# Performance work log

Measured on AMD Instinct MI355X. Metric: run time of the kernel, lower is better.

## Reference

```python
import math
import jax, jax.numpy as jnp
import numpy as np

B, S, E, H = 1, 2048, 2048, 16
HD = E // H // 2            # qk head dim = 64
DEPTH = 12
LAMBDA_INIT = 0.8 - 0.6 * math.exp(-0.3 * DEPTH)
EPS = 1e-5
NEG = -1e30

# rotary table (non-learned buffer), interleaved pairs, dim = HD
_pos = np.arange(S, dtype=np.float32)[:, None]
_div = np.exp(np.arange(0, HD, 2, dtype=np.float32) * (-math.log(10000.0) / HD))
COS = jnp.asarray(np.cos(_pos * _div))  # [S, HD/2]
SIN = jnp.asarray(np.sin(_pos * _div))


def _rope_interleaved(x):
    # x: [B, S, nH, HD]; rotate interleaved pairs (x0,x1),(x2,x3),...
    x1 = x[..., 0::2]
    x2 = x[..., 1::2]
    c = COS[None, :, None, :]
    s = SIN[None, :, None, :]
    o1 = x1 * c - x2 * s
    o2 = x1 * s + x2 * c
    return jnp.stack([o1, o2], axis=-1).reshape(x.shape)


def _causal_attn(q, k, v):
    # q,k: [B,S,H,Dk]; v: [B,S,H,Dv]; flash_attn default scale = Dk**-0.5
    scale = q.shape[-1] ** -0.5
    scores = jnp.einsum('bqhd,bkhd->bhqk', q, k) * scale
    mask = jnp.tril(jnp.ones((S, S), dtype=bool))
    scores = jnp.where(mask[None, None], scores, NEG)
    p = jax.nn.softmax(scores, axis=-1)
    return jnp.einsum('bhqk,bkhd->bqhd', p, v)


def setup_inputs() -> dict:
    key = jax.random.key(0)
    ks = jax.random.split(key, 10)
    w = lambda k: jax.random.normal(k, (E, E), dtype=jnp.float32) * 0.02
    lam = lambda k: jax.random.normal(k, (HD,), dtype=jnp.float32) * 0.1
    return {
        'x': jax.random.normal(ks[0], (B, S, E), dtype=jnp.float32),
        'Wq': w(ks[1]), 'Wk': w(ks[2]), 'Wv': w(ks[3]), 'Wo': w(ks[4]),
        'lq1': lam(ks[5]), 'lk1': lam(ks[6]), 'lq2': lam(ks[7]), 'lk2': lam(ks[8]),
        'g': jnp.ones((2 * HD,), dtype=jnp.float32),  # RMSNorm affine weight
    }


def reference(x, Wq, Wk, Wv, Wo, lq1, lk1, lq2, lk2, g):
    q = (x @ Wq).reshape(B, S, 2 * H, HD)
    k = (x @ Wk).reshape(B, S, 2 * H, HD)
    v = (x @ Wv).reshape(B, S, H, 2 * HD)
    q = _rope_interleaved(q).reshape(B, S, H, 2, HD)
    k = _rope_interleaved(k).reshape(B, S, H, 2, HD)
    q1, q2 = q[:, :, :, 0], q[:, :, :, 1]
    k1, k2 = k[:, :, :, 0], k[:, :, :, 1]
    attn1 = _causal_attn(q1, k1, v)  # [B,S,H,2*HD]
    attn2 = _causal_attn(q2, k2, v)
    lambda_full = (jnp.exp(jnp.sum(lq1 * lk1)) - jnp.exp(jnp.sum(lq2 * lk2))
                   + LAMBDA_INIT)
    a = attn1 - lambda_full * attn2
    # RMSNorm over last dim (2*HD) with affine weight g
    a = a * jax.lax.rsqrt(jnp.mean(a * a, axis=-1, keepdims=True) + EPS) * g
    a = a * (1.0 - LAMBDA_INIT)
    a = a.reshape(B, S, E)
    return a @ Wo
```

## Files before the change

kernel.cpp:

```cpp
#include <hip/hip_runtime.h>

typedef unsigned short u16;
typedef __bf16 bf16x8 __attribute__((ext_vector_type(8)));
typedef float f32x4 __attribute__((ext_vector_type(4)));

#define LAMBDA_INIT_F 0.7836057665f
#define ONE_MINUS_LI  0.2163942335f
#define Q_PRESCALE 0.1803368801f

__device__ __forceinline__ u16 f2bf(float f) {
  union { float f; unsigned u; } v; v.f = f;
  unsigned r = v.u + 0x7fffu + ((v.u >> 16) & 1u);
  return (u16)(r >> 16);
}

__device__ __forceinline__ float fast_exp2(float x) {
#if __has_builtin(__builtin_amdgcn_exp2f)
  return __builtin_amdgcn_exp2f(x);
#else
  return __builtin_exp2f(x);
#endif
}

__device__ __forceinline__ void gload_lds16(const void* g, void* l) {
  __builtin_amdgcn_global_load_lds(
      (const __attribute__((address_space(1))) void*)g,
      (__attribute__((address_space(3))) void*)l, 16, 0, 0);
}

__global__ __launch_bounds__(256) void prep_kernel(
    const float* __restrict__ x, const float* __restrict__ Wq,
    const float* __restrict__ Wk, const float* __restrict__ Wv,
    const float* __restrict__ Wo, const float* __restrict__ lq1,
    const float* __restrict__ lk1, const float* __restrict__ lq2,
    const float* __restrict__ lk2, u16* __restrict__ xb,
    u16* __restrict__ WqkvT, u16* __restrict__ WoT,
    float* __restrict__ cosT, float* __restrict__ sinT, float* __restrict__ lam) {
  __shared__ float t[32][33];
  const int bid = blockIdx.x;
  const int tid = threadIdx.x;
  if (bid < 16384) {
    const int z = bid >> 12;
    const int rem = bid & 4095;
    const int n0 = (rem & 63) * 32, k0 = (rem >> 6) * 32;
    const float* src = (z == 0) ? Wq : (z == 1) ? Wk : (z == 2) ? Wv : Wo;
    const int tx = tid & 31, ty = tid >> 5;
#pragma unroll
    for (int i = 0; i < 4; ++i)
      t[ty + i * 8][tx] = src[(size_t)(k0 + ty + i * 8) * 2048 + n0 + tx];
    __syncthreads();
    u16* dst = (z < 3) ? (WqkvT + ((size_t)z * 2048 + n0) * 2048 + k0)
                       : (WoT + (size_t)n0 * 2048 + k0);
#pragma unroll
    for (int i = 0; i < 4; ++i)
      dst[(size_t)(ty + i * 8) * 2048 + tx] = f2bf(t[tx][ty + i * 8]);
  } else if (bid < 16384 + 4096) {
    const int i = ((bid - 16384) * 256 + tid) * 4;
    const float4 v = *(const float4*)(x + i);
    u16 tmp[4] = {f2bf(v.x), f2bf(v.y), f2bf(v.z), f2bf(v.w)};
    *(uint2*)(xb + i) = *(const uint2*)tmp;
  } else if (bid < 16384 + 4096 + 256) {
    const int idx = (bid - 16384 - 4096) * 256 + tid;
    const int s = idx >> 5, i = idx & 31;
    const float div = expf((float)(2 * i) * (-9.210340371976184f / 64.f));
    const float ang = (float)s * div;
    cosT[idx] = cosf(ang);
    sinT[idx] = sinf(ang);
  } else {
    if (tid < 64) {
      float p1 = lq1[tid] * lk1[tid];
      float p2 = lq2[tid] * lk2[tid];
#pragma unroll
      for (int mk = 1; mk < 64; mk <<= 1) {
        p1 += __shfl_xor(p1, mk);
        p2 += __shfl_xor(p2, mk);
      }
      if (tid == 0) *lam = expf(p1) - expf(p2) + LAMBDA_INIT_F;
    }
  }
}

__global__ __launch_bounds__(256) void gemm_bt_kernel(
    const u16* __restrict__ A, const u16* __restrict__ Bt,
    float* __restrict__ C, int M, int N, int K, int mode,
    const float* __restrict__ cosT, const float* __restrict__ sinT,
    u16* __restrict__ Qh, u16* __restrict__ Kh, u16* __restrict__ Vt) {
  __shared__ u16 As[2][128 * 64];
  __shared__ u16 Bs[2][128 * 64];
  const int tid = threadIdx.x;
  const int lane = tid & 63;
  const int w = tid >> 6;
  const int wm = w >> 1, wn = w & 1;
  const long m0 = (long)blockIdx.y * 128;
  const long n0 = (long)blockIdx.x * 128;

  f32x4 acc[4][4];
#pragma unroll
  for (int i = 0; i < 4; ++i)
#pragma unroll
    for (int j = 0; j < 4; ++j) acc[i][j] = f32x4{0.f, 0.f, 0.f, 0.f};

  const int sr = lane >> 3;
  const int scS = ((lane & 7) ^ sr) * 8;
  const int fr = lane & 15;
  const int kgrp = lane >> 4;
  const int swz = (fr & 7) << 3;

  const u16* aSrc = A + (m0 + w * 32 + sr) * (long)K + scS;
  const u16* bSrc = Bt + (n0 + w * 32 + sr) * (long)K + scS;

  auto stage = [&](int b, long koff) {
#pragma unroll
    for (int g = 0; g < 4; ++g) {
      gload_lds16(aSrc + koff + (size_t)g * 8 * K, &As[b][(w * 32 + g * 8) * 64]);
      gload_lds16(bSrc + koff + (size_t)g * 8 * K, &Bs[b][(w * 32 + g * 8) * 64]);
    }
  };

  stage(0, 0);
  __syncthreads();
  int cur = 0;
  for (int k0 = 0; k0 < K; k0 += 64) {
    if (k0 + 64 < K) stage(cur ^ 1, k0 + 64);
    __builtin_amdgcn_s_setprio(1);
#pragma unroll
    for (int ks = 0; ks < 2; ++ks) {
      bf16x8 af[4], bfr[4];
#pragma unroll
      for (int mi = 0; mi < 4; ++mi)
        af[mi] = *(const bf16x8*)&As[cur][(wm * 64 + mi * 16 + fr) * 64 +
                                          ((ks * 32 + kgrp * 8) ^ swz)];
#pragma unroll
      for (int ni = 0; ni < 4; ++ni)
        bfr[ni] = *(const bf16x8*)&Bs[cur][(wn * 64 + ni * 16 + fr) * 64 +
                                           ((ks * 32 + kgrp * 8) ^ swz)];
#pragma unroll
      for (int mi = 0; mi < 4; ++mi)
#pragma unroll
        for (int ni = 0; ni < 4; ++ni)
          acc[mi][ni] =
              __builtin_amdgcn_mfma_f32_16x16x32_bf16(af[mi], bfr[ni], acc[mi][ni], 0, 0, 0);
    }
    __builtin_amdgcn_s_setprio(0);
    __syncthreads();
    cur ^= 1;
  }
  const int rg = (lane >> 4) * 4;
  if (mode == 0) {
#pragma unroll
    for (int mi = 0; mi < 4; ++mi)
#pragma unroll
      for (int ni = 0; ni < 4; ++ni) {
        const long col = n0 + wn * 64 + ni * 16 + fr;
#pragma unroll
        for (int j = 0; j < 4; ++j) {
          const long row = m0 + wm * 64 + mi * 16 + rg + j;
          C[row * N + col] = acc[mi][ni][j];
        }
      }
  } else if (n0 >= 4096) {
#pragma unroll
    for (int mi = 0; mi < 4; ++mi)
#pragma unroll
      for (int ni = 0; ni < 4; ++ni) {
        const long vr = n0 - 4096 + wn * 64 + ni * 16 + fr;
#pragma unroll
        for (int j = 0; j < 4; ++j) {
          const long row = m0 + wm * 64 + mi * 16 + rg + j;
          Vt[vr * 2048 + row] = f2bf(acc[mi][ni][j]);
        }
      }
  } else {
    const int isK = (int)(n0 >> 11);
    u16* dstBase = isK ? Kh : Qh;
    const float scl = isK ? 1.0f : Q_PRESCALE;
#pragma unroll
    for (int mi = 0; mi < 4; ++mi)
#pragma unroll
      for (int ni = 0; ni < 4; ++ni) {
        const int col = (int)(n0 & 2047) + wn * 64 + ni * 16 + fr;
        const int hh = col >> 6, d = col & 63, i2 = (col & 63) >> 1;
        const bool odd = d & 1;
#pragma unroll
        for (int j = 0; j < 4; ++j) {
          const int row = (int)m0 + wm * 64 + mi * 16 + rg + j;
          const float v = acc[mi][ni][j];
          const float p = __shfl_xor(v, 1);
          const float c = cosT[row * 32 + i2], sn = sinT[row * 32 + i2];
          const float outv = odd ? (p * sn + v * c) : (v * c - p * sn);
          dstBase[((size_t)hh * 2048 + row) * 64 + d] = f2bf(outv * scl);
        }
      }
  }
}

__global__ __launch_bounds__(256) void attn_kernel(
    const u16* __restrict__ Qh, const u16* __restrict__ Kh,
    const u16* __restrict__ Vt, float* __restrict__ attnOut) {
  __shared__ u16 Kt[2][64 * 64];
  __shared__ u16 Vs[2][128 * 64];
  __shared__ __bf16 Ps[4 * 16 * 64];
  const int tid = threadIdx.x, lane = tid & 63, w = tid >> 6;
  const int fr = lane & 15, kgrp = lane >> 4;
  const int bid = blockIdx.x;
  const int xcd = bid & 7, idx = bid >> 3;
  const int hh = xcd * 4 + (idx & 3);
  const int pairIdx = idx >> 2;
  const int h = hh >> 1, comp = hh & 1;
  const int q0A = pairIdx * 64, q0B = (31 - pairIdx) * 64;
  const int jmaxA = pairIdx, jmaxB = 31 - pairIdx;
  const int ntA = jmaxA + 1, ntot = ntA + jmaxB + 1;

  const int sr = lane >> 3;
  const int scS = (((lane & 7) ^ sr) * 8);
  const int swz = (fr & 7) << 3;

  bf16x8 qf0, qf1;
  {
    const u16* qb = Qh + ((size_t)hh * 2048 + q0A + w * 16 + fr) * 64 + kgrp * 8;
    qf0 = *(const bf16x8*)qb;
    qf1 = *(const bf16x8*)(qb + 32);
  }
  bf16x8 onesf;
#pragma unroll
  for (int i = 0; i < 8; ++i) onesf[i] = (__bf16)1.0f;

  f32x4 o[9];
#pragma unroll
  for (int i = 0; i < 9; ++i) o[i] = f32x4{0.f, 0.f, 0.f, 0.f};
  float m_r[4] = {-1e30f, -1e30f, -1e30f, -1e30f};

  auto stage = [&](int b, int kv0) {
#pragma unroll
    for (int i = 0; i < 2; ++i)
      gload_lds16(Kh + ((size_t)hh * 2048 + kv0 + i * 32 + w * 8 + sr) * 64 + scS,
                  &Kt[b][(i * 32 + w * 8) * 64]);
#pragma unroll
    for (int i = 0; i < 4; ++i)
      gload_lds16(Vt + ((size_t)h * 128 + i * 32 + w * 8 + sr) * 2048 + kv0 + scS,
                  &Vs[b][(i * 32 + w * 8) * 64]);
  };

  auto writeOut = [&](int q0) {
    float* outp = attnOut + (size_t)comp * (2048 * 2048);
#pragma unroll
    for (int j = 0; j < 4; ++j) {
      const int row = q0 + w * 16 + kgrp * 4 + j;
      const float inv = 1.0f / o[8][j];
      float* op = outp + (size_t)row * 2048 + h * 128;
#pragma unroll
      for (int nf = 0; nf < 8; ++nf) op[nf * 16 + fr] = o[nf][j] * inv;
    }
  };

  stage(0, 0);
  __syncthreads();

  for (int t = 0; t < ntot; ++t) {
    const int cur = t & 1;
    if (t + 1 < ntot) {
      const int nk = (t + 1 < ntA) ? (t + 1) * 64 : (t + 1 - ntA) * 64;
      stage(cur ^ 1, nk);
    }
    const bool inA = t < ntA;
    const int q0 = inA ? q0A : q0B;
    const int jj = inA ? t : t - ntA;
    const int kv0 = jj * 64;
    const bool diag = inA ? (jj == jmaxA) : (jj == jmaxB);

    f32x4 s[4];
    __builtin_amdgcn_s_setprio(1);
#pragma unroll
    for (int nf = 0; nf < 4; ++nf) {
      s[nf] = f32x4{0.f, 0.f, 0.f, 0.f};
      const bf16x8 b0 = *(const bf16x8*)&Kt[cur][(nf * 16 + fr) * 64 + ((kgrp * 8) ^ swz)];
      const bf16x8 b1 =
          *(const bf16x8*)&Kt[cur][(nf * 16 + fr) * 64 + ((32 + kgrp * 8) ^ swz)];
      s[nf] = __builtin_amdgcn_mfma_f32_16x16x32_bf16(qf0, b0, s[nf], 0, 0, 0);
      s[nf] = __builtin_amdgcn_mfma_f32_16x16x32_bf16(qf1, b1, s[nf], 0, 0, 0);
    }
    __builtin_amdgcn_s_setprio(0);

    float pmax[4] = {-1e30f, -1e30f, -1e30f, -1e30f};
    if (diag) {
#pragma unroll
      for (int nf = 0; nf < 4; ++nf) {
        const int key = kv0 + nf * 16 + fr;
#pragma unroll
        for (int j = 0; j < 4; ++j) {
          float sc2 = s[nf][j];
          if (key > q0 + w * 16 + kgrp * 4 + j) sc2 = -1e30f;
          s[nf][j] = sc2;
          pmax[j] = fmaxf(pmax[j], sc2);
        }
      }
    } else {
#pragma unroll
      for (int nf = 0; nf < 4; ++nf)
#pragma unroll
        for (int j = 0; j < 4; ++j) pmax[j] = fmaxf(pmax[j], s[nf][j]);
    }
#pragma unroll
    for (int j = 0; j < 4; ++j)
#pragma unroll
      for (int mk = 1; mk < 16; mk <<= 1) pmax[j] = fmaxf(pmax[j], __shfl_xor(pmax[j], mk));

    bool grow = false;
#pragma unroll
    for (int j = 0; j < 4; ++j) grow |= (pmax[j] > m_r[j]);
    if (__any(grow)) {
#pragma unroll
      for (int j = 0; j < 4; ++j) {
        const float mn = fmaxf(m_r[j], pmax[j]);
        const float sf = fast_exp2(m_r[j] - mn);
        m_r[j] = mn;
#pragma unroll
        for (int nf = 0; nf < 9; ++nf) o[nf][j] *= sf;
      }
    }

#pragma unroll
    for (int nf = 0; nf < 4; ++nf)
#pragma unroll
      for (int j = 0; j < 4; ++j) {
        const float p = fast_exp2(s[nf][j] - m_r[j]);
        const int prow = kgrp * 4 + j;
        Ps[w * 1024 + prow * 64 + ((nf * 16 + fr) ^ ((prow & 7) << 3))] = (__bf16)p;
      }

    const bf16x8 pa0 = *(const bf16x8*)&Ps[w * 1024 + fr * 64 + ((kgrp * 8) ^ swz)];
    const bf16x8 pa1 = *(const bf16x8*)&Ps[w * 1024 + fr * 64 + ((32 + kgrp * 8) ^ swz)];
    __builtin_amdgcn_s_setprio(1);
#pragma unroll
    for (int nf = 0; nf < 8; ++nf) {
      const bf16x8 v0 = *(const bf16x8*)&Vs[cur][(nf * 16 + fr) * 64 + ((kgrp * 8) ^ swz)];
      const bf16x8 v1 =
          *(const bf16x8*)&Vs[cur][(nf * 16 + fr) * 64 + ((32 + kgrp * 8) ^ swz)];
      o[nf] = __builtin_amdgcn_mfma_f32_16x16x32_bf16(pa0, v0, o[nf], 0, 0, 0);
      o[nf] = __builtin_amdgcn_mfma_f32_16x16x32_bf16(pa1, v1, o[nf], 0, 0, 0);
    }
    o[8] = __builtin_amdgcn_mfma_f32_16x16x32_bf16(pa0, onesf, o[8], 0, 0, 0);
    o[8] = __builtin_amdgcn_mfma_f32_16x16x32_bf16(pa1, onesf, o[8], 0, 0, 0);
    __builtin_amdgcn_s_setprio(0);

    if (t == jmaxA) {
      writeOut(q0A);
#pragma unroll
      for (int i = 0; i < 9; ++i) o[i] = f32x4{0.f, 0.f, 0.f, 0.f};
#pragma unroll
      for (int j = 0; j < 4; ++j) m_r[j] = -1e30f;
      const u16* qb = Qh + ((size_t)hh * 2048 + q0B + w * 16 + fr) * 64 + kgrp * 8;
      qf0 = *(const bf16x8*)qb;
      qf1 = *(const bf16x8*)(qb + 32);
    }
    __syncthreads();
  }
  writeOut(q0B);
}

__global__ __launch_bounds__(256) void combine_kernel(
    const float* __restrict__ attn, const float* __restrict__ lam,
    const float* __restrict__ g, u16* __restrict__ ab) {
  const int lane = threadIdx.x & 63;
  const int idx = blockIdx.x * 4 + (threadIdx.x >> 6);
  const int s = idx >> 4, h = idx & 15;
  const float lf = *lam;
  const float* a1 = attn + (size_t)s * 2048 + h * 128;
  const float* a2 = a1 + (size_t)2048 * 2048;
  const float x0 = a1[lane] - lf * a2[lane];
  const float x1 = a1[lane + 64] - lf * a2[lane + 64];
  float ss = x0 * x0 + x1 * x1;
#pragma unroll
  for (int mk = 1; mk < 64; mk <<= 1) ss += __shfl_xor(ss, mk);
  const float r = rsqrtf(ss * (1.0f / 128.0f) + 1e-5f) * ONE_MINUS_LI;
  u16* op = ab + (size_t)s * 2048 + h * 128;
  op[lane] = f2bf(x0 * r * g[lane]);
  op[lane + 64] = f2bf(x1 * r * g[lane + 64]);
}

extern "C" void kernel_launch(void* const* d_in, const int* in_sizes, int n_in,
                              void* d_out, int out_size, void* d_ws, size_t ws_size,
                              hipStream_t stream) {
  const float* x = (const float*)d_in[0];
  const float* Wq = (const float*)d_in[1];
  const float* Wk = (const float*)d_in[2];
  const float* Wv = (const float*)d_in[3];
  const float* Wo = (const float*)d_in[4];
  const float* lq1 = (const float*)d_in[5];
  const float* lk1 = (const float*)d_in[6];
  const float* lq2 = (const float*)d_in[7];
  const float* lk2 = (const float*)d_in[8];
  const float* g = (const float*)d_in[9];
  float* out = (float*)d_out;

  char* ws = (char*)d_ws;
  u16* xb = (u16*)(ws);
  u16* WqkvT = (u16*)(ws + (size_t)(8u << 20));
  u16* WoT = (u16*)(ws + (size_t)(32u << 20));
  float* attn = (float*)(ws + (size_t)(40u << 20));
  u16* Qh = (u16*)(ws + (size_t)(88u << 20));
  u16* Kh = (u16*)(ws + (size_t)(96u << 20));
  u16* Vt = (u16*)(ws + (size_t)(104u << 20));
  u16* ab = (u16*)(ws + (size_t)(112u << 20));
  float* cosT = (float*)(ws + (size_t)(120u << 20));
  float* sinT = (float*)(ws + (size_t)(120u << 20) + (256u << 10));
  float* lam = (float*)(ws + (size_t)(120u << 20) + (512u << 10));

  prep_kernel<<<16384 + 4096 + 256 + 1, 256, 0, stream>>>(
      x, Wq, Wk, Wv, Wo, lq1, lk1, lq2, lk2, xb, WqkvT, WoT, cosT, sinT, lam);
  gemm_bt_kernel<<<dim3(48, 16), 256, 0, stream>>>(xb, WqkvT, nullptr, 2048, 6144, 2048,
                                                   1, cosT, sinT, Qh, Kh, Vt);
  attn_kernel<<<512, 256, 0, stream>>>(Qh, Kh, Vt, attn);
  combine_kernel<<<8192, 256, 0, stream>>>(attn, lam, g, ab);
  gemm_bt_kernel<<<dim3(16, 16), 256, 0, stream>>>(ab, WoT, out, 2048, 2048, 2048,
                                                   0, nullptr, nullptr, nullptr, nullptr,
                                                   nullptr);
}
```

Baseline: 316.0 us.

## Fuse differential combine and RMSNorm into attention kernel, sharing V across components

The attention kernel now runs both differential components of a head in one 512-thread block: waves 0-3 compute component 1 and waves 4-7 compute component 2, and the V tile is staged once and shared. Component 2 passes its normalized output through shared memory so component 1 can apply the lambda subtraction, RMSNorm and gain, then write bf16 directly. This removes the separate combine kernel and the 32 MB fp32 intermediate round trip, and halves V loads. In exchange the grid drops to 256 larger blocks, shared memory use rises, and block-level syncs gain extra work at the switch points.

```diff
diff --git a/kernel.cpp b/kernel.cpp
--- a/kernel.cpp
+++ b/kernel.cpp
@@ -194,30 +194,39 @@
   }
 }
 
-__global__ __launch_bounds__(256) void attn_kernel(
+__global__ __launch_bounds__(512) void attn_kernel(
     const u16* __restrict__ Qh, const u16* __restrict__ Kh,
-    const u16* __restrict__ Vt, float* __restrict__ attnOut) {
-  __shared__ u16 Kt[2][64 * 64];
+    const u16* __restrict__ Vt, const float* __restrict__ lam,
+    const float* __restrict__ g, u16* __restrict__ ab) {
+  __shared__ u16 Kt1[2][64 * 64];
+  __shared__ u16 Kt2[2][64 * 64];
   __shared__ u16 Vs[2][128 * 64];
-  __shared__ __bf16 Ps[4 * 16 * 64];
+  __shared__ __bf16 Ps[8 * 16 * 64];
+  __shared__ float Xch[4][16][132];
   const int tid = threadIdx.x, lane = tid & 63, w = tid >> 6;
+  const int comp = w >> 2, wq = w & 3;
   const int fr = lane & 15, kgrp = lane >> 4;
   const int bid = blockIdx.x;
   const int xcd = bid & 7, idx = bid >> 3;
-  const int hh = xcd * 4 + (idx & 3);
-  const int pairIdx = idx >> 2;
-  const int h = hh >> 1, comp = hh & 1;
+  const int h = xcd * 2 + (idx & 1);
+  const int pairIdx = idx >> 1;
   const int q0A = pairIdx * 64, q0B = (31 - pairIdx) * 64;
   const int jmaxA = pairIdx, jmaxB = 31 - pairIdx;
   const int ntA = jmaxA + 1, ntot = ntA + jmaxB + 1;
+  const size_t hhQ = (size_t)(2 * h + comp);
 
   const int sr = lane >> 3;
   const int scS = (((lane & 7) ^ sr) * 8);
   const int swz = (fr & 7) << 3;
 
+  const float lf = *lam;
+  float gv[8];
+#pragma unroll
+  for (int nf = 0; nf < 8; ++nf) gv[nf] = g[nf * 16 + fr];
+
   bf16x8 qf0, qf1;
   {
-    const u16* qb = Qh + ((size_t)hh * 2048 + q0A + w * 16 + fr) * 64 + kgrp * 8;
+    const u16* qb = Qh + (hhQ * 2048 + q0A + wq * 16 + fr) * 64 + kgrp * 8;
     qf0 = *(const bf16x8*)qb;
     qf1 = *(const bf16x8*)(qb + 32);
   }
@@ -231,26 +240,49 @@
   float m_r[4] = {-1e30f, -1e30f, -1e30f, -1e30f};
 
   auto stage = [&](int b, int kv0) {
+    gload_lds16(Kh + ((size_t)(2 * h) * 2048 + kv0 + w * 8 + sr) * 64 + scS,
+                &Kt1[b][(w * 8) * 64]);
+    gload_lds16(Kh + ((size_t)(2 * h + 1) * 2048 + kv0 + w * 8 + sr) * 64 + scS,
+                &Kt2[b][(w * 8) * 64]);
 #pragma unroll
     for (int i = 0; i < 2; ++i)
-      gload_lds16(Kh + ((size_t)hh * 2048 + kv0 + i * 32 + w * 8 + sr) * 64 + scS,
-                  &Kt[b][(i * 32 + w * 8) * 64]);
-#pragma unroll
-    for (int i = 0; i < 4; ++i)
-      gload_lds16(Vt + ((size_t)h * 128 + i * 32 + w * 8 + sr) * 2048 + kv0 + scS,
-                  &Vs[b][(i * 32 + w * 8) * 64]);
+      gload_lds16(Vt + ((size_t)h * 128 + w * 16 + i * 8 + sr) * 2048 + kv0 + scS,
+                  &Vs[b][(w * 16 + i * 8) * 64]);
   };
 
-  auto writeOut = [&](int q0) {
-    float* outp = attnOut + (size_t)comp * (2048 * 2048);
+  auto publish = [&]() {
 #pragma unroll
     for (int j = 0; j < 4; ++j) {
-      const int row = q0 + w * 16 + kgrp * 4 + j;
       const float inv = 1.0f / o[8][j];
-      float* op = outp + (size_t)row * 2048 + h * 128;
-#pragma unroll
-      for (int nf = 0; nf < 8; ++nf) op[nf * 16 + fr] = o[nf][j] * inv;
-    }
+#pragma unroll
+      for (int nf = 0; nf < 8; ++nf)
+        Xch[wq][kgrp * 4 + j][nf * 16 + fr] = o[nf][j] * inv;
+    }
+  };
+  auto combineStore = [&](int q0) {
+#pragma unroll
+    for (int j = 0; j < 4; ++j) {
+      const float inv = 1.0f / o[8][j];
+      const int row = q0 + wq * 16 + kgrp * 4 + j;
+      float xv[8], ss = 0.f;
+#pragma unroll
+      for (int nf = 0; nf < 8; ++nf) {
+        xv[nf] = o[nf][j] * inv - lf * Xch[wq][kgrp * 4 + j][nf * 16 + fr];
+        ss += xv[nf] * xv[nf];
+      }
+#pragma unroll
+      for (int mk = 1; mk < 16; mk <<= 1) ss += __shfl_xor(ss, mk);
+      const float r = rsqrtf(ss * (1.0f / 128.0f) + 1e-5f) * ONE_MINUS_LI;
+      u16* op = ab + (size_t)row * 2048 + h * 128;
+#pragma unroll
+      for (int nf = 0; nf < 8; ++nf) op[nf * 16 + fr] = f2bf(xv[nf] * r * gv[nf]);
+    }
+  };
+  auto resetState = [&]() {
+#pragma unroll
+    for (int i = 0; i < 9; ++i) o[i] = f32x4{0.f, 0.f, 0.f, 0.f};
+#pragma unroll
+    for (int j = 0; j < 4; ++j) m_r[j] = -1e30f;
   };
 
   stage(0, 0);
@@ -267,15 +299,15 @@
     const int jj = inA ? t : t - ntA;
     const int kv0 = jj * 64;
     const bool diag = inA ? (jj == jmaxA) : (jj == jmaxB);
+    const u16* kt = comp ? &Kt2[cur][0] : &Kt1[cur][0];
 
     f32x4 s[4];
     __builtin_amdgcn_s_setprio(1);
 #pragma unroll
     for (int nf = 0; nf < 4; ++nf) {
       s[nf] = f32x4{0.f, 0.f, 0.f, 0.f};
-      const bf16x8 b0 = *(const bf16x8*)&Kt[cur][(nf * 16 + fr) * 64 + ((kgrp * 8) ^ swz)];
-      const bf16x8 b1 =
-          *(const bf16x8*)&Kt[cur][(nf * 16 + fr) * 64 + ((32 + kgrp * 8) ^ swz)];
+      const bf16x8 b0 = *(const bf16x8*)&kt[(nf * 16 + fr) * 64 + ((kgrp * 8) ^ swz)];
+      const bf16x8 b1 = *(const bf16x8*)&kt[(nf * 16 + fr) * 64 + ((32 + kgrp * 8) ^ swz)];
       s[nf] = __builtin_amdgcn_mfma_f32_16x16x32_bf16(qf0, b0, s[nf], 0, 0, 0);
       s[nf] = __builtin_amdgcn_mfma_f32_16x16x32_bf16(qf1, b1, s[nf], 0, 0, 0);
     }
@@ -289,7 +321,7 @@
 #pragma unroll
         for (int j = 0; j < 4; ++j) {
           float sc2 = s[nf][j];
-          if (key > q0 + w * 16 + kgrp * 4 + j) sc2 = -1e30f;
+          if (key > q0 + wq * 16 + kgrp * 4 + j) sc2 = -1e30f;
           s[nf][j] = sc2;
           pmax[j] = fmaxf(pmax[j], sc2);
         }
@@ -343,39 +375,19 @@
     o[8] = __builtin_amdgcn_mfma_f32_16x16x32_bf16(pa1, onesf, o[8], 0, 0, 0);
     __builtin_amdgcn_s_setprio(0);
 
+    if (t == jmaxA && comp == 1) publish();
+    __syncthreads();
     if (t == jmaxA) {
-      writeOut(q0A);
-#pragma unroll
-      for (int i = 0; i < 9; ++i) o[i] = f32x4{0.f, 0.f, 0.f, 0.f};
-#pragma unroll
-      for (int j = 0; j < 4; ++j) m_r[j] = -1e30f;
-      const u16* qb = Qh + ((size_t)hh * 2048 + q0B + w * 16 + fr) * 64 + kgrp * 8;
+      if (comp == 0) combineStore(q0A);
+      resetState();
+      const u16* qb = Qh + (hhQ * 2048 + q0B + wq * 16 + fr) * 64 + kgrp * 8;
       qf0 = *(const bf16x8*)qb;
       qf1 = *(const bf16x8*)(qb + 32);
     }
-    __syncthreads();
   }
-  writeOut(q0B);
-}
-
-__global__ __launch_bounds__(256) void combine_kernel(
-    const float* __restrict__ attn, const float* __restrict__ lam,
-    const float* __restrict__ g, u16* __restrict__ ab) {
-  const int lane = threadIdx.x & 63;
-  const int idx = blockIdx.x * 4 + (threadIdx.x >> 6);
-  const int s = idx >> 4, h = idx & 15;
-  const float lf = *lam;
-  const float* a1 = attn + (size_t)s * 2048 + h * 128;
-  const float* a2 = a1 + (size_t)2048 * 2048;
-  const float x0 = a1[lane] - lf * a2[lane];
-  const float x1 = a1[lane + 64] - lf * a2[lane + 64];
-  float ss = x0 * x0 + x1 * x1;
-#pragma unroll
-  for (int mk = 1; mk < 64; mk <<= 1) ss += __shfl_xor(ss, mk);
-  const float r = rsqrtf(ss * (1.0f / 128.0f) + 1e-5f) * ONE_MINUS_LI;
-  u16* op = ab + (size_t)s * 2048 + h * 128;
-  op[lane] = f2bf(x0 * r * g[lane]);
-  op[lane + 64] = f2bf(x1 * r * g[lane + 64]);
+  if (comp == 1) publish();
+  __syncthreads();
+  if (comp == 0) combineStore(q0B);
 }
 
 extern "C" void kernel_launch(void* const* d_in, const int* in_sizes, int n_in,
@@ -397,7 +409,6 @@
   u16* xb = (u16*)(ws);
   u16* WqkvT = (u16*)(ws + (size_t)(8u << 20));
   u16* WoT = (u16*)(ws + (size_t)(32u << 20));
-  float* attn = (float*)(ws + (size_t)(40u << 20));
   u16* Qh = (u16*)(ws + (size_t)(88u << 20));
   u16* Kh = (u16*)(ws + (size_t)(96u << 20));
   u16* Vt = (u16*)(ws + (size_t)(104u << 20));
@@ -410,8 +421,7 @@
       x, Wq, Wk, Wv, Wo, lq1, lk1, lq2, lk2, xb, WqkvT, WoT, cosT, sinT, lam);
   gemm_bt_kernel<<<dim3(48, 16), 256, 0, stream>>>(xb, WqkvT, nullptr, 2048, 6144, 2048,
                                                    1, cosT, sinT, Qh, Kh, Vt);
-  attn_kernel<<<512, 256, 0, stream>>>(Qh, Kh, Vt, attn);
-  combine_kernel<<<8192, 256, 0, stream>>>(attn, lam, g, ab);
+  attn_kernel<<<256, 512, 0, stream>>>(Qh, Kh, Vt, lam, g, ab);
   gemm_bt_kernel<<<dim3(16, 16), 256, 0, stream>>>(ab, WoT, out, 2048, 2048, 2048,
                                                    0, nullptr, nullptr, nullptr, nullptr,
                                                    nullptr);
```

Measured after the change: 308.2 us. 2.4% less time.
